# Kernel optimization log

Measured on AMD Instinct MI355X. Metric: run time of the kernel, lower is better.

Reference implementation:

```python
import jax, jax.numpy as jnp
import numpy as np

B, T, V, E, H, C = 64, 512, 30000, 256, 512, 9


def setup_inputs() -> dict:
    key = jax.random.key(0)
    ks = jax.random.split(key, 12)
    s = 0.05
    x = jax.random.randint(ks[0], (B, T), 0, V, dtype=jnp.int32)
    seq_len = jax.random.randint(ks[1], (B,), T // 2, T + 1, dtype=jnp.int32)
    y = jax.random.randint(ks[2], (B, T), 0, C, dtype=jnp.int32)
    emb = jax.random.normal(ks[3], (V, E), jnp.float32) * s
    def lstm_p(k):
        k1, k2, k3 = jax.random.split(k, 3)
        return (jax.random.normal(k1, (4 * H, E), jnp.float32) * s,
                jax.random.normal(k2, (4 * H, H), jnp.float32) * s,
                jax.random.normal(k3, (4 * H,), jnp.float32) * s)
    Wih_f, Whh_f, b_f = lstm_p(ks[4])
    Wih_b, Whh_b, b_b = lstm_p(ks[5])
    Wfc = jax.random.normal(ks[6], (C, 2 * H), jnp.float32) * s
    start_t = jax.random.normal(ks[7], (C,), jnp.float32) * 0.1
    end_t = jax.random.normal(ks[8], (C,), jnp.float32) * 0.1
    trans = jax.random.normal(ks[9], (C, C), jnp.float32) * 0.1
    return dict(x=x, seq_len=seq_len, y=y, emb=emb, Wih_f=Wih_f, Whh_f=Whh_f,
                b_f=b_f, Wih_b=Wih_b, Whh_b=Whh_b, b_b=b_b, Wfc=Wfc,
                start_t=start_t, end_t=end_t, trans=trans)


def _lstm_dir(xt, mt, Wih, Whh, b, reverse):
    # xt: [T,B,E], mt: [T,B,1] bool. State frozen at padded steps (= packed-seq semantics).
    h0 = jnp.zeros((xt.shape[1], Whh.shape[1]), xt.dtype)
    def step(carry, inp):
        h, c = carry
        x_t, m_t = inp
        g = x_t @ Wih.T + h @ Whh.T + b
        i, f, gg, o = jnp.split(g, 4, axis=-1)  # torch gate order i,f,g,o
        c_new = jax.nn.sigmoid(f) * c + jax.nn.sigmoid(i) * jnp.tanh(gg)
        h_new = jax.nn.sigmoid(o) * jnp.tanh(c_new)
        return (jnp.where(m_t, h_new, h), jnp.where(m_t, c_new, c)), h_new
    _, hs = jax.lax.scan(step, (h0, h0), (xt, mt), reverse=reverse)
    return hs  # [T,B,H]


def reference(x, seq_len, y, emb, Wih_f, Whh_f, b_f, Wih_b, Whh_b, b_b, Wfc,
              start_t, end_t, trans):
    mask = jnp.arange(T)[None, :] < seq_len[:, None]  # [B,T]
    xt = emb[x].transpose(1, 0, 2)                    # [T,B,E]
    mt = mask.T[:, :, None]
    hf = _lstm_dir(xt, mt, Wih_f, Whh_f, b_f, False)
    hb = _lstm_dir(xt, mt, Wih_b, Whh_b, b_b, True)
    out = jnp.concatenate([hf, hb], -1).transpose(1, 0, 2)  # [B,T,2H]
    out = out * mask[:, :, None]                             # pad_packed zeros
    emis = jax.nn.log_softmax(out @ Wfc.T, axis=-1)          # [B,T,C]
    maskf = mask.astype(emis.dtype)
    # --- CRF numerator (gold-path score) ---
    em_sc = jnp.take_along_axis(emis, y[..., None], -1)[..., 0] * maskf
    tr_sc = trans[y[:, :-1], y[:, 1:]] * maskf[:, 1:]
    last_tag = jnp.take_along_axis(y, (seq_len - 1)[:, None], 1)[:, 0]
    num = start_t[y[:, 0]] + em_sc.sum(-1) + tr_sc.sum(-1) + end_t[last_tag]
    # --- CRF denominator (log partition, forward algorithm) ---
    score0 = start_t[None, :] + emis[:, 0]  # [B,C]
    def step(score, inp):
        em_t, m_t = inp  # [B,C], [B]
        nxt = jax.scipy.special.logsumexp(
            score[:, :, None] + trans[None] + em_t[:, None, :], axis=1)
        return jnp.where(m_t[:, None], nxt, score), None
    score, _ = jax.lax.scan(step, score0,
                            (emis.transpose(1, 0, 2)[1:], mask.T[1:]))
    den = jax.scipy.special.logsumexp(score + end_t[None, :], axis=1)
    return -(num - den).sum()  # -sum log-likelihood
```

## Files before the change

kernel.cpp:

```cpp
#include <hip/hip_runtime.h>
#include <hip/hip_bf16.h>


using short8 = __attribute__((ext_vector_type(8))) short;
using f32x4  = __attribute__((ext_vector_type(4))) float;
using i32x4  = __attribute__((ext_vector_type(4))) int;

#define TT 512
#define BB 64

__device__ __forceinline__ unsigned short f2bf(float f) {
  unsigned int u = __builtin_bit_cast(unsigned int, f);
  u += 0x7FFFu + ((u >> 16) & 1u);
  return (unsigned short)(u >> 16);
}
__device__ __forceinline__ float bf2f(short s) {
  unsigned int u = ((unsigned int)(unsigned short)s) << 16;
  return __builtin_bit_cast(float, u);
}
__device__ __forceinline__ float fast_rcp(float x) { return __builtin_amdgcn_rcpf(x); }
__device__ __forceinline__ float sigmoid_f(float x) { return fast_rcp(1.f + __expf(-x)); }
__device__ __forceinline__ float tanh_f(float x) {
  float e = __expf(-2.f * fabsf(x));
  float r = (1.f - e) * fast_rcp(1.f + e);
  return copysignf(r, x);
}

__device__ __forceinline__ i32x4 load16_sc(const void* p) {
  i32x4 r;
  asm volatile("global_load_dwordx4 %0, %1, off sc0 sc1" : "=v"(r) : "v"(p));
  return r;
}
__device__ __forceinline__ i32x4 load16_sc_wait(const void* p) {
  i32x4 r;
  asm volatile("global_load_dwordx4 %0, %1, off sc0 sc1\n\ts_waitcnt vmcnt(0)"
               : "=v"(r) : "v"(p) : "memory");
  return r;
}
__device__ __forceinline__ void store4_sc(void* p, unsigned int v) {
  asm volatile("global_store_dword %0, %1, off sc0 sc1" :: "v"(p), "v"(v) : "memory");
}
#define WAITV(n) do { asm volatile("s_waitcnt vmcnt(" #n ")" ::: "memory"); \
                      __builtin_amdgcn_sched_barrier(0); } while (0)

__global__ void pack_weights(const float* __restrict__ Wih_f, const float* __restrict__ Whh_f,
                             const float* __restrict__ Wih_b, const float* __restrict__ Whh_b,
                             const float* __restrict__ Wfc,
                             short* __restrict__ WpackX, short* __restrict__ WpackH,
                             short* __restrict__ WfcPack) {
  const int bid = blockIdx.x;
  const int d = bid & 1, sl = bid >> 1;
  const float* Wih = d ? Wih_b : Wih_f;
  const float* Whh = d ? Whh_b : Whh_f;
  for (int idx = threadIdx.x; idx < 64 * 256; idx += 256) {
    int n = idx >> 8, k = idx & 255;
    int nt = n >> 5, mi = (n >> 4) & 1, u = (n >> 2) & 3, g = n & 3;
    int r = g * 512 + sl * 16 + nt * 8 + 2 * u + mi;
    WpackX[((size_t)bid * 64 + n) * 256 + k] = (short)f2bf(Wih[(size_t)r * 256 + k]);
  }
  for (int idx = threadIdx.x; idx < 64 * 512; idx += 256) {
    int n = idx >> 9, k = idx & 511;
    int nt = n >> 5, mi = (n >> 4) & 1, u = (n >> 2) & 3, g = n & 3;
    int r = g * 512 + sl * 16 + nt * 8 + 2 * u + mi;
    WpackH[((size_t)bid * 64 + n) * 512 + k] = (short)f2bf(Whh[(size_t)r * 512 + k]);
  }
  if (bid == 0) {
    for (int idx = threadIdx.x; idx < 16 * 1024; idx += 256) {
      int c = idx >> 10, k = idx & 1023;
      WfcPack[idx] = (c < 9) ? (short)f2bf(Wfc[c * 1024 + k]) : (short)0;
    }
  }
}

__global__ void pack_x(const int* __restrict__ x, const float* __restrict__ emb,
                       short* __restrict__ xpack) {
  int gid = blockIdx.x * 256 + threadIdx.x;
  int lane = gid & 63;
  int kc = (gid >> 6) & 7;
  int mt = (gid >> 9) & 3;
  int t  = gid >> 11;
  int b  = mt * 16 + (lane & 15);
  int k0 = kc * 32 + (lane >> 4) * 8;
  int vid = x[b * TT + t];
  const float* e = emb + (size_t)vid * 256 + k0;
  short8 v;
#pragma unroll
  for (int i = 0; i < 8; ++i) v[i] = (short)f2bf(e[i]);
  *reinterpret_cast<short8*>(xpack + (size_t)gid * 8) = v;
}

__global__ void init_state(int* __restrict__ flags) {
  flags[threadIdx.x] = 0;
}

__launch_bounds__(256, 1)
__global__ void lstm_step_kernel(const short8* __restrict__ xpack,
                                 const short* __restrict__ WpackX,
                                 const short* __restrict__ WpackH,
                                 short* __restrict__ hexch,
                                 int* __restrict__ flags,
                                 const float* __restrict__ b_f,
                                 const float* __restrict__ b_b,
                                 const int* __restrict__ seq_len) {
  const int bid = blockIdx.x;
  const int d = bid & 1;
  const int sl = bid >> 1;
  const int tid = threadIdx.x;
  const int wv = tid >> 6;
  const int lane = tid & 63;
  const int l15 = lane & 15;
  const int lhi = lane >> 4;
  const int mtb = wv & 1;
  const int nt = wv >> 1;
  const int mbase = mtb * 32;
  const int nbase = nt * 32;
  const int ubase = sl * 16 + nt * 8;
  const int kc_w  = ubase >> 5;
  const int lhi_c = (ubase >> 3) & 3;

  short8 bfx[2][8];
#pragma unroll
  for (int mi = 0; mi < 2; ++mi)
#pragma unroll
    for (int kc = 0; kc < 8; ++kc)
      bfx[mi][kc] = *reinterpret_cast<const short8*>(
          WpackX + ((size_t)bid * 64 + nbase + mi * 16 + l15) * 256 + kc * 32 + lhi * 8);
  short8 bfh[2][16];
#pragma unroll
  for (int mi = 0; mi < 2; ++mi)
#pragma unroll
    for (int kc = 0; kc < 16; ++kc)
      bfh[mi][kc] = *reinterpret_cast<const short8*>(
          WpackH + ((size_t)bid * 64 + nbase + mi * 16 + l15) * 512 + kc * 32 + lhi * 8);

  const float* bias = d ? b_b : b_f;
  float b4[2][4];
#pragma unroll
  for (int mi = 0; mi < 2; ++mi) {
    int jg = ubase + 2 * lhi + mi;
#pragma unroll
    for (int g = 0; g < 4; ++g) b4[mi][g] = bias[g * 512 + jg];
  }
  int Lr[2];
#pragma unroll
  for (int ni = 0; ni < 2; ++ni)
    Lr[ni] = seq_len[mbase + ni * 16 + l15];
  float cst[2][2] = {{0.f, 0.f}, {0.f, 0.f}};
  float hst[2][2] = {{0.f, 0.f}, {0.f, 0.f}};

  int* fl_grp  = flags + (d * 2 + mtb) * 64;
  int* fl_mine = fl_grp + (sl * 2 + nt);
  const int* fl_quad = fl_grp + (lane & 15) * 4;

  for (int s = 0; s < TT; ++s) {
    const int t = d ? (TT - 1 - s) : s;
    f32x4 acc[2][2];
#pragma unroll
    for (int mi = 0; mi < 2; ++mi)
#pragma unroll
      for (int ni = 0; ni < 2; ++ni) acc[mi][ni] = (f32x4){0.f, 0.f, 0.f, 0.f};

    const short8* xp = xpack + (size_t)t * 2048;
#pragma unroll
    for (int kc = 0; kc < 8; ++kc) {
      short8 bf[2];
#pragma unroll
      for (int ni = 0; ni < 2; ++ni)
        bf[ni] = xp[((mtb * 2 + ni) * 8 + kc) * 64 + lane];
#pragma unroll
      for (int mi = 0; mi < 2; ++mi)
#pragma unroll
        for (int ni = 0; ni < 2; ++ni)
          acc[mi][ni] = __builtin_amdgcn_mfma_f32_16x16x32_bf16(bfx[mi][kc], bf[ni], acc[mi][ni], 0, 0, 0);
    }

    if (s > 0) {
      {
        int vtries = 0;
        while (true) {
          i32x4 f = load16_sc_wait(fl_quad);
          bool ok = (f[0] >= s) & (f[1] >= s) & (f[2] >= s) & (f[3] >= s);
          if (__all(ok)) break;
          __builtin_amdgcn_s_sleep(1);
          if (++vtries > (1 << 18)) break;
        }
      }
      __builtin_amdgcn_sched_barrier(0);

      const int tprev = d ? (t + 1) : (t - 1);
      const i32x4* hp16 = (const i32x4*)(hexch + ((size_t)d * TT + tprev) * 32768);
      i32x4 hbuf[32];
#pragma unroll
      for (int kc = 0; kc < 16; ++kc)
#pragma unroll
        for (int ni = 0; ni < 2; ++ni)
          hbuf[kc * 2 + ni] =
              load16_sc(hp16 + ((mtb * 16 + kc) * 2 + ni) * 64 + lane);
      WAITV(16);
#pragma unroll
      for (int kc = 0; kc < 8; ++kc)
#pragma unroll
        for (int ni = 0; ni < 2; ++ni) {
          short8 b = __builtin_bit_cast(short8, hbuf[kc * 2 + ni]);
#pragma unroll
          for (int mi = 0; mi < 2; ++mi)
            acc[mi][ni] = __builtin_amdgcn_mfma_f32_16x16x32_bf16(bfh[mi][kc], b, acc[mi][ni], 0, 0, 0);
        }
      WAITV(0);
#pragma unroll
      for (int kc = 8; kc < 16; ++kc)
#pragma unroll
        for (int ni = 0; ni < 2; ++ni) {
          short8 b = __builtin_bit_cast(short8, hbuf[kc * 2 + ni]);
#pragma unroll
          for (int mi = 0; mi < 2; ++mi)
            acc[mi][ni] = __builtin_amdgcn_mfma_f32_16x16x32_bf16(bfh[mi][kc], b, acc[mi][ni], 0, 0, 0);
        }
    }

    short* hx = hexch + ((size_t)d * TT + t) * 32768;
#pragma unroll
    for (int ni = 0; ni < 2; ++ni) {
      const bool m = (t < Lr[ni]);
      unsigned short hnb[2];
#pragma unroll
      for (int mi = 0; mi < 2; ++mi) {
        f32x4 A = acc[mi][ni];
        float gi = A[0] + b4[mi][0];
        float gf = A[1] + b4[mi][1];
        float gg = A[2] + b4[mi][2];
        float go = A[3] + b4[mi][3];
        float si = sigmoid_f(gi), sf = sigmoid_f(gf), so = sigmoid_f(go);
        float ct = sf * cst[mi][ni] + si * tanh_f(gg);
        float ht = so * tanh_f(ct);
        float cn = m ? ct : cst[mi][ni];
        float hn = m ? ht : hst[mi][ni];
        cst[mi][ni] = cn;
        hst[mi][ni] = hn;
        hnb[mi] = f2bf(hn);
      }
      unsigned int up = ((unsigned int)hnb[1] << 16) | hnb[0];
      store4_sc((char*)hx
                    + (size_t)(((mtb * 16 + kc_w) * 2 + ni) * 64 + lhi_c * 16 + l15) * 16
                    + lhi * 4,
                up);
    }

    if (lane == 0) {
      int sv = s + 1;
      asm volatile("s_waitcnt vmcnt(0)\n\t"
                   "global_store_dword %0, %1, off sc0 sc1"
                   :: "v"(fl_mine), "v"(sv) : "memory");
    }
  }
}

__launch_bounds__(256)
__global__ void emis_kernel(const short* __restrict__ hexch,
                            const short* __restrict__ WfcPack,
                            float* __restrict__ logits) {
  __shared__ short wfc[16 * 1032];
  const int tid = threadIdx.x;
  for (int idx = tid; idx < 2048; idx += 256) {
    int n = idx >> 7, c8 = idx & 127;
    short8 v = *reinterpret_cast<const short8*>(WfcPack + n * 1024 + c8 * 8);
    *reinterpret_cast<short8*>(&wfc[n * 1032 + c8 * 8]) = v;
  }
  __syncthreads();
  const int wv = tid >> 6, lane = tid & 63;
  const int l15 = lane & 15, lhi = lane >> 4;
  const i32x4* hx = (const i32x4*)hexch;
#pragma unroll
  for (int mt2 = 0; mt2 < 2; ++mt2) {
    int m = (blockIdx.x * 4 + wv) * 2 + mt2;
    int r0 = m * 16;
    int t   = r0 >> 6;
    int mtb = (r0 >> 5) & 1;
    int ti  = (r0 >> 4) & 1;
    f32x4 acc = (f32x4){0.f, 0.f, 0.f, 0.f};
#pragma unroll
    for (int kc = 0; kc < 32; ++kc) {
      int dd  = kc >> 4;
      int kcf = kc & 15;
      short8 a = __builtin_bit_cast(short8,
          hx[((size_t)dd * TT + t) * 4096 + ((mtb * 16 + kcf) * 2 + ti) * 64
             + lhi * 16 + l15]);
      short8 b = *reinterpret_cast<const short8*>(&wfc[l15 * 1032 + kc * 32 + lhi * 8]);
      acc = __builtin_amdgcn_mfma_f32_16x16x32_bf16(a, b, acc, 0, 0, 0);
    }
    int c = l15;
    if (c < 9) {
#pragma unroll
      for (int reg = 0; reg < 4; ++reg) {
        int rr = r0 + lhi * 4 + reg;
        int b = rr & 63, tt = rr >> 6;
        logits[((size_t)b * TT + tt) * 9 + c] = acc[reg];
      }
    }
  }
}

__global__ void crf_kernel(const float* __restrict__ logits, const int* __restrict__ y,
                           const int* __restrict__ seq_len, const float* __restrict__ start_t,
                           const float* __restrict__ end_t, const float* __restrict__ trans,
                           float* __restrict__ partials) {
  const int b = blockIdx.x;
  const int lane = threadIdx.x;
  const float* lg = logits + (size_t)b * TT * 9;
  const int* yb = y + b * TT;
  const int L = seq_len[b];

  float acc = 0.f;
  for (int t = lane; t < TT; t += 64) {
    if (t < L) {
      float mx = lg[t * 9];
      for (int c = 1; c < 9; ++c) mx = fmaxf(mx, lg[t * 9 + c]);
      float se = 0.f;
      for (int c = 0; c < 9; ++c) se += __expf(lg[t * 9 + c] - mx);
      float lse = mx + __logf(se);
      int yt = yb[t];
      acc += lg[t * 9 + yt] - lse;
      if (t >= 1) acc += trans[yb[t - 1] * 9 + yt];
    }
  }
#pragma unroll
  for (int off = 32; off >= 1; off >>= 1) acc += __shfl_down(acc, off, 64);

  const int c = (lane < 9) ? lane : 0;
  float score;
  {
    float mx = lg[0];
    for (int cc = 1; cc < 9; ++cc) mx = fmaxf(mx, lg[cc]);
    float se = 0.f;
    for (int cc = 0; cc < 9; ++cc) se += __expf(lg[cc] - mx);
    score = start_t[c] + lg[c] - (mx + __logf(se));
  }
  float tr[9];
#pragma unroll
  for (int cc = 0; cc < 9; ++cc) tr[cc] = trans[cc * 9 + c];
  for (int t = 1; t < L; ++t) {
    const float* lt = lg + t * 9;
    float mx2 = lt[0];
    for (int cc = 1; cc < 9; ++cc) mx2 = fmaxf(mx2, lt[cc]);
    float se2 = 0.f;
    for (int cc = 0; cc < 9; ++cc) se2 += __expf(lt[cc] - mx2);
    float em = lt[c] - (mx2 + __logf(se2));
    float vv[9];
    float mx = -1e30f;
#pragma unroll
    for (int cc = 0; cc < 9; ++cc) {
      float sp = __shfl(score, cc, 64);
      vv[cc] = sp + tr[cc];
      mx = fmaxf(mx, vv[cc]);
    }
    float se = 0.f;
#pragma unroll
    for (int cc = 0; cc < 9; ++cc) se += __expf(vv[cc] - mx);
    score = mx + __logf(se) + em;
  }
  float val = (lane < 9) ? (score + end_t[lane]) : -1e30f;
  float mm = val;
#pragma unroll
  for (int off = 1; off < 64; off <<= 1) mm = fmaxf(mm, __shfl_xor(mm, off, 64));
  float se = (lane < 9) ? __expf(val - mm) : 0.f;
#pragma unroll
  for (int off = 1; off < 64; off <<= 1) se += __shfl_xor(se, off, 64);
  float den = mm + __logf(se);
  if (lane == 0) {
    float num = acc + start_t[yb[0]] + end_t[yb[L - 1]];
    partials[b] = num - den;
  }
}

__global__ void finalize_kernel(const float* __restrict__ partials, float* __restrict__ out) {
  int l = threadIdx.x;
  float v = partials[l];
#pragma unroll
  for (int off = 32; off >= 1; off >>= 1) v += __shfl_down(v, off, 64);
  if (l == 0) out[0] = -v;
}

extern "C" void kernel_launch(void* const* d_in, const int* in_sizes, int n_in,
                              void* d_out, int out_size, void* d_ws, size_t ws_size,
                              hipStream_t stream) {
  const int*   x     = (const int*)d_in[0];
  const int*   seqln = (const int*)d_in[1];
  const int*   y     = (const int*)d_in[2];
  const float* emb   = (const float*)d_in[3];
  const float* Wih_f = (const float*)d_in[4];
  const float* Whh_f = (const float*)d_in[5];
  const float* b_f   = (const float*)d_in[6];
  const float* Wih_b = (const float*)d_in[7];
  const float* Whh_b = (const float*)d_in[8];
  const float* b_b   = (const float*)d_in[9];
  const float* Wfc   = (const float*)d_in[10];
  const float* st    = (const float*)d_in[11];
  const float* en    = (const float*)d_in[12];
  const float* trans = (const float*)d_in[13];
  float* out = (float*)d_out;

  char* ws = (char*)d_ws;
  short* WpackX   = (short*)(ws + 0);
  short* WpackH   = (short*)(ws + 2097152);
  short* WfcPack  = (short*)(ws + 6291456);
  short* xpack    = (short*)(ws + 6324224);
  int*   flags    = (int*)  (ws + 23101440);
  float* partials = (float*)(ws + 23102464);
  float* logits   = (float*)(ws + 23102720);
  short* hexch    = (short*)(ws + 24282368);

  pack_weights<<<64, 256, 0, stream>>>(Wih_f, Whh_f, Wih_b, Whh_b, Wfc,
                                       WpackX, WpackH, WfcPack);
  pack_x<<<4096, 256, 0, stream>>>(x, emb, xpack);
  init_state<<<1, 256, 0, stream>>>(flags);
  lstm_step_kernel<<<64, 256, 0, stream>>>((const short8*)xpack, WpackX, WpackH,
                                           hexch, flags, b_f, b_b, seqln);
  emis_kernel<<<256, 256, 0, stream>>>(hexch, WfcPack, logits);
  crf_kernel<<<64, 64, 0, stream>>>(logits, y, seqln, st, en, trans, partials);
  finalize_kernel<<<1, 64, 0, stream>>>(partials, out);
}
```

Before: 3.242 ms.

## Replace flag-based step sync with sentinel-validated speculative hidden-state loads

Fills the hidden-state exchange buffer with a NaN-pattern sentinel before the LSTM kernel. Each step now issues its loads of the previous hidden state speculatively before the input MFMAs, checks them for the sentinel, and falls back to flag polling plus selective reloads only when stale data is found. It also drops the vmcnt wait before publishing the step flag. This aims to take the flag round-trip off the serial recurrence critical path, at the cost of an extra 64MB fill kernel and reliance on 16-byte store/load atomicity and on the sentinel never matching real bf16 data.

```diff
diff --git a/kernel.cpp b/kernel.cpp
--- a/kernel.cpp
+++ b/kernel.cpp
@@ -8,6 +8,7 @@
 
 #define TT 512
 #define BB 64
+#define SENTW ((int)0x7FC07FC0)
 
 __device__ __forceinline__ unsigned short f2bf(float f) {
   unsigned int u = __builtin_bit_cast(unsigned int, f);
@@ -91,6 +92,11 @@
 
 __global__ void init_state(int* __restrict__ flags) {
   flags[threadIdx.x] = 0;
+}
+__global__ void sentinel_fill(i32x4* __restrict__ p) {
+  int gid = blockIdx.x * 256 + threadIdx.x;
+  const i32x4 v = {SENTW, SENTW, SENTW, SENTW};
+  for (int i = gid; i < 4194304; i += 4096 * 256) p[i] = v;
 }
 
 __launch_bounds__(256, 1)
@@ -152,6 +158,19 @@
   int* fl_mine = fl_grp + (sl * 2 + nt);
   const int* fl_quad = fl_grp + (lane & 15) * 4;
 
+#define HADDR16(kc, ni) (hp16 + ((mtb * 16 + (kc)) * 2 + (ni)) * 64 + lane)
+#define VALIDATE(badv)                                                          \
+  do {                                                                          \
+    badv = 0u;                                                                  \
+    _Pragma("unroll")                                                           \
+    for (int k = 0; k < 32; ++k) {                                              \
+      i32x4 v = hbuf[k];                                                        \
+      bool bb = (v[0] == SENTW) | (v[1] == SENTW) |                             \
+                (v[2] == SENTW) | (v[3] == SENTW);                              \
+      badv |= (bb ? (1u << k) : 0u);                                            \
+    }                                                                           \
+  } while (0)
+
   for (int s = 0; s < TT; ++s) {
     const int t = d ? (TT - 1 - s) : s;
     f32x4 acc[2][2];
@@ -160,6 +179,18 @@
 #pragma unroll
       for (int ni = 0; ni < 2; ++ni) acc[mi][ni] = (f32x4){0.f, 0.f, 0.f, 0.f};
 
+    i32x4 hbuf[32];
+    const i32x4* hp16 = nullptr;
+    if (s > 0) {
+      const int tprev = d ? (t + 1) : (t - 1);
+      hp16 = (const i32x4*)(hexch + ((size_t)d * TT + tprev) * 32768);
+#pragma unroll
+      for (int kc = 0; kc < 16; ++kc)
+#pragma unroll
+        for (int ni = 0; ni < 2; ++ni)
+          hbuf[kc * 2 + ni] = load16_sc(HADDR16(kc, ni));
+    }
+
     const short8* xp = xpack + (size_t)t * 2048;
 #pragma unroll
     for (int kc = 0; kc < 8; ++kc) {
@@ -175,7 +206,10 @@
     }
 
     if (s > 0) {
-      {
+      WAITV(0);
+      unsigned bad;
+      VALIDATE(bad);
+      if (__any(bad != 0u)) {
         int vtries = 0;
         while (true) {
           i32x4 f = load16_sc_wait(fl_quad);
@@ -184,31 +218,23 @@
           __builtin_amdgcn_s_sleep(1);
           if (++vtries > (1 << 18)) break;
         }
+        int tries = 0;
+        do {
+#pragma unroll
+          for (int kc = 0; kc < 16; ++kc)
+#pragma unroll
+            for (int ni = 0; ni < 2; ++ni) {
+              const int k = kc * 2 + ni;
+              if (bad & (1u << k)) hbuf[k] = load16_sc(HADDR16(kc, ni));
+            }
+          WAITV(0);
+          VALIDATE(bad);
+        } while (__any(bad != 0u) && ++tries < (1 << 16));
       }
       __builtin_amdgcn_sched_barrier(0);
 
-      const int tprev = d ? (t + 1) : (t - 1);
-      const i32x4* hp16 = (const i32x4*)(hexch + ((size_t)d * TT + tprev) * 32768);
-      i32x4 hbuf[32];
 #pragma unroll
       for (int kc = 0; kc < 16; ++kc)
-#pragma unroll
-        for (int ni = 0; ni < 2; ++ni)
-          hbuf[kc * 2 + ni] =
-              load16_sc(hp16 + ((mtb * 16 + kc) * 2 + ni) * 64 + lane);
-      WAITV(16);
-#pragma unroll
-      for (int kc = 0; kc < 8; ++kc)
-#pragma unroll
-        for (int ni = 0; ni < 2; ++ni) {
-          short8 b = __builtin_bit_cast(short8, hbuf[kc * 2 + ni]);
-#pragma unroll
-          for (int mi = 0; mi < 2; ++mi)
-            acc[mi][ni] = __builtin_amdgcn_mfma_f32_16x16x32_bf16(bfh[mi][kc], b, acc[mi][ni], 0, 0, 0);
-        }
-      WAITV(0);
-#pragma unroll
-      for (int kc = 8; kc < 16; ++kc)
 #pragma unroll
         for (int ni = 0; ni < 2; ++ni) {
           short8 b = __builtin_bit_cast(short8, hbuf[kc * 2 + ni]);
@@ -248,11 +274,12 @@
 
     if (lane == 0) {
       int sv = s + 1;
-      asm volatile("s_waitcnt vmcnt(0)\n\t"
-                   "global_store_dword %0, %1, off sc0 sc1"
+      asm volatile("global_store_dword %0, %1, off sc0 sc1"
                    :: "v"(fl_mine), "v"(sv) : "memory");
     }
   }
+#undef HADDR16
+#undef VALIDATE
 }
 
 __launch_bounds__(256)
@@ -413,6 +440,7 @@
                                        WpackX, WpackH, WfcPack);
   pack_x<<<4096, 256, 0, stream>>>(x, emb, xpack);
   init_state<<<1, 256, 0, stream>>>(flags);
+  sentinel_fill<<<4096, 256, 0, stream>>>((i32x4*)hexch);
   lstm_step_kernel<<<64, 256, 0, stream>>>((const short8*)xpack, WpackX, WpackH,
                                            hexch, flags, b_f, b_b, seqln);
   emis_kernel<<<256, 256, 0, stream>>>(hexch, WfcPack, logits);
```

After: 4.634 ms. 1.43x slower.
